# Optimization experiments

Hardware: AMD Instinct MI355X
Metric: run time of the kernel (lower is better)

The kernel has to match this reference:

```python
import jax, jax.numpy as jnp
import numpy as np

K = 3  # == stride, neighbors per token


def setup_inputs() -> dict:
    key = jax.random.key(0)
    k1, k2, k3 = jax.random.split(key, 3)
    x = jax.random.normal(k1, (16, 64, 2048), dtype=jnp.float32)        # (B, C, T)
    W = jax.random.normal(k2, (64, 64, K), dtype=jnp.float32) * 0.05     # (O, I, K) conv1d weight
    b = jax.random.normal(k3, (64,), dtype=jnp.float32) * 0.05           # (O,) conv1d bias
    return {"x": x, "W": W, "b": b}


def reference(x, W, b):
    B, C, T = x.shape
    # pairwise squared euclidean distances over the channel dim: (B, T, T)
    nsq = jnp.sum(x * x, axis=1)                       # (B, T)
    dot = jnp.einsum('bct,bcs->bts', x, x)             # (B, T, T)
    dist = jnp.maximum(nsq[:, :, None] + nsq[:, None, :] - 2.0 * dot, 0.0)
    # K nearest neighbors (smallest distance -> top_k of negated dist)
    _, idx = jax.lax.top_k(-dist, K)                   # (B, T, K) int32 indices
    # gather neighbor features: prime[b, c, i*K + k] = x[b, c, idx[b, i, k]]
    idx_flat = idx.reshape(B, 1, T * K)
    prime = jnp.take_along_axis(x, jnp.broadcast_to(idx_flat, (B, C, T * K)), axis=2)
    # Conv1d with kernel_size=K, stride=K, padding=0 -> output length T
    out = jax.lax.conv_general_dilated(
        prime, W, window_strides=(K,), padding='VALID',
        dimension_numbers=('NCH', 'OIH', 'NCH'))
    return out + b[None, :, None]
```

## Files before the change

### kernel.cpp

```cpp
#include <hip/hip_runtime.h>

#define B_ 16
#define C_ 64
#define T_ 2048
#define O_ 64
#define KNN 3
#define HSPLIT 2
#define JCH (T_ / HSPLIT)

typedef short short8   __attribute__((ext_vector_type(8)));
typedef float f32x4    __attribute__((ext_vector_type(4)));
typedef unsigned short ushortx4 __attribute__((ext_vector_type(4)));

#define XT_OFF 0
#define XS_OFF (XT_OFF + B_ * T_ * C_)
#define NSQ_OFF (XS_OFF + B_ * T_ * C_)
#define WT_OFF (NSQ_OFF + B_ * T_)
#define CAND_OFF (WT_OFF + 192 * O_)

__device__ inline ushort bf16_rne(float f) {
    union { float f; unsigned u; } cv; cv.f = f;
    unsigned u = cv.u;
    u += 0x7FFF + ((u >> 16) & 1);
    return (ushort)(u >> 16);
}
__device__ inline float bf16_val(ushort h) {
    union { unsigned u; float f; } cv; cv.u = ((unsigned)h) << 16; return cv.f;
}

__global__ __launch_bounds__(256) void prep_kernel(const float* __restrict__ x,
                                                   const float* __restrict__ W,
                                                   float* __restrict__ ws) {
    float*  xT  = ws + XT_OFF;
    ushort* xs  = (ushort*)(ws + XS_OFF);
    float*  nsq = ws + NSQ_OFF;
    float*  Wt  = ws + WT_OFF;
    int blk = blockIdx.x;
    int tid = threadIdx.x;
    if (blk < B_ * (T_ / 64)) {
        int b  = blk / (T_ / 64);
        int t0 = (blk % (T_ / 64)) * 64;
        __shared__ float tl[64 * 65];
        #pragma unroll
        for (int r = 0; r < 16; ++r) {
            int e = r * 256 + tid;
            int c = e >> 6, t = e & 63;
            tl[c * 65 + t] = x[(b * C_ + c) * T_ + t0 + t];
        }
        __syncthreads();
        #pragma unroll
        for (int r = 0; r < 16; ++r) {
            int e = r * 256 + tid;
            int t = e >> 6, c = e & 63;
            float v = tl[c * 65 + t];
            size_t rowg = (size_t)(b * T_ + t0 + t);
            xT[rowg * 64 + c] = v;
            ushort hi = bf16_rne(v);
            float  fr = v - bf16_val(hi);
            ushort lo = bf16_rne(fr);
            xs[rowg * 128 + c]      = hi;
            xs[rowg * 128 + 64 + c] = lo;
        }
        if (tid < 64) {
            float s = 0.f;
            #pragma unroll
            for (int c = 0; c < 64; ++c) { float v = tl[c * 65 + tid]; s = fmaf(v, v, s); }
            nsq[b * T_ + t0 + tid] = s;
        }
    } else {
        int e = (blk - B_ * (T_ / 64)) * 256 + tid;
        if (e < O_ * C_ * KNN) {
            int o = e / (C_ * KNN);
            int c = (e / KNN) % C_;
            int k = e % KNN;
            Wt[(k * 64 + c) * O_ + o] = W[e];
        }
    }
}

__global__ __launch_bounds__(256, 4) void knn_mfma_kernel(const ushort* __restrict__ xs,
                                                          const float* __restrict__ nsq,
                                                          ushort* __restrict__ cand) {
    __shared__ __align__(16) ushort jbuf[2][32 * 128];
    __shared__ float nsqs[JCH];

    int bid = blockIdx.x;
    int g   = bid & 31;
    int m   = bid >> 5;
    int b   = g >> 1, h = g & 1;
    int i0  = m * 128;
    int tid = threadIdx.x;
    int w   = tid >> 6, l = tid & 63, lr = l & 15, lq = l >> 4;
    const ushort* xsb = xs + (size_t)b * T_ * 128;
    int jBase = h * JCH;

    ((float4*)nsqs)[tid] = ((const float4*)(nsq + b * T_ + jBase))[tid];

    short8 bA0, bA1, bA4, bA5, bB0, bB1, bB4, bB5;
    {
        const ushort* ia = xsb + (size_t)(i0 + w * 32 + lr) * 128 + lq * 8;
        bA0 = *(const short8*)(ia + 0);  bA1 = *(const short8*)(ia + 32);
        bA4 = *(const short8*)(ia + 64); bA5 = *(const short8*)(ia + 96);
        const ushort* ib2 = ia + 16 * 128;
        bB0 = *(const short8*)(ib2 + 0);  bB1 = *(const short8*)(ib2 + 32);
        bB4 = *(const short8*)(ib2 + 64); bB5 = *(const short8*)(ib2 + 96);
    }
    float niA = nsq[b * T_ + i0 + w * 32 + lr] + 4.0f;
    float niB = nsq[b * T_ + i0 + w * 32 + 16 + lr] + 4.0f;

    const float INF = __builtin_inff();
    float kA0 = INF, kA1 = INF, kA2 = INF, kA3 = INF;
    float kB0 = INF, kB1 = INF, kB2 = INF, kB3 = INF;

    int cSw = lr ^ (w * 4 + lq);
    #define ISSUE_DMA(jsv, bufv) {                                               \
        _Pragma("unroll")                                                        \
        for (int p = 0; p < 2; ++p) {                                            \
            int rloc = p * 16 + w * 4 + lq;                                      \
            const ushort* gp = xsb + (size_t)(jBase + (jsv) * 32 + rloc) * 128 + cSw * 8; \
            __builtin_amdgcn_global_load_lds(                                    \
                (const __attribute__((address_space(1))) void*)gp,               \
                (__attribute__((address_space(3))) void*)(jbuf[bufv] + (p * 16 + w * 4) * 128), \
                16, 0, 0);                                                       \
        } }

    ISSUE_DMA(0, 0);

    #pragma unroll 1
    for (int js = 0; js < 32; ++js) {
        asm volatile("s_waitcnt vmcnt(0)" ::: "memory");
        __syncthreads();
        if (js < 31) ISSUE_DMA(js + 1, (js + 1) & 1);
        const char* jb8 = (const char*)jbuf[js & 1];
        #pragma unroll
        for (int tile = 0; tile < 2; ++tile) {
            const char* rowp = jb8 + (tile * 16 + lr) * 256;
            short8 ah0 = *(const short8*)(rowp + ((( 0 + lq) ^ lr) << 4));
            short8 ah1 = *(const short8*)(rowp + ((( 4 + lq) ^ lr) << 4));
            short8 al0 = *(const short8*)(rowp + ((( 8 + lq) ^ lr) << 4));
            short8 al1 = *(const short8*)(rowp + (((12 + lq) ^ lr) << 4));
            f32x4 accA = {0.f, 0.f, 0.f, 0.f};
            f32x4 accB = {0.f, 0.f, 0.f, 0.f};
            accA = __builtin_amdgcn_mfma_f32_16x16x32_bf16(ah0, bA0, accA, 0, 0, 0);
            accB = __builtin_amdgcn_mfma_f32_16x16x32_bf16(ah0, bB0, accB, 0, 0, 0);
            accA = __builtin_amdgcn_mfma_f32_16x16x32_bf16(ah1, bA1, accA, 0, 0, 0);
            accB = __builtin_amdgcn_mfma_f32_16x16x32_bf16(ah1, bB1, accB, 0, 0, 0);
            accA = __builtin_amdgcn_mfma_f32_16x16x32_bf16(al0, bA0, accA, 0, 0, 0);
            accB = __builtin_amdgcn_mfma_f32_16x16x32_bf16(al0, bB0, accB, 0, 0, 0);
            accA = __builtin_amdgcn_mfma_f32_16x16x32_bf16(al1, bA1, accA, 0, 0, 0);
            accB = __builtin_amdgcn_mfma_f32_16x16x32_bf16(al1, bB1, accB, 0, 0, 0);
            accA = __builtin_amdgcn_mfma_f32_16x16x32_bf16(ah0, bA4, accA, 0, 0, 0);
            accB = __builtin_amdgcn_mfma_f32_16x16x32_bf16(ah0, bB4, accB, 0, 0, 0);
            accA = __builtin_amdgcn_mfma_f32_16x16x32_bf16(ah1, bA5, accA, 0, 0, 0);
            accB = __builtin_amdgcn_mfma_f32_16x16x32_bf16(ah1, bB5, accB, 0, 0, 0);
            float4 nv = *(const float4*)(nsqs + js * 32 + tile * 16 + lq * 4);
            int idb = ((js * 2 + tile) << 2) | (lq << 8);
            #define INS(K0, K1, K2, K3, sv, idv) {                                  \
                unsigned uu = (__float_as_uint(sv) & 0xFFFFFC00u) | (unsigned)(idv); \
                float kf = __uint_as_float(uu);                                      \
                float n0 = fminf(K0, kf);                                            \
                float n1 = __builtin_amdgcn_fmed3f(K0, K1, kf);                      \
                float n2 = __builtin_amdgcn_fmed3f(K1, K2, kf);                      \
                float n3 = __builtin_amdgcn_fmed3f(K2, K3, kf);                      \
                K0 = n0; K1 = n1; K2 = n2; K3 = n3; }
            {
                float s0 = fmaf(-2.f, accA[0], nv.x + niA); INS(kA0, kA1, kA2, kA3, s0, idb + 0);
                float s1 = fmaf(-2.f, accA[1], nv.y + niA); INS(kA0, kA1, kA2, kA3, s1, idb + 1);
                float s2 = fmaf(-2.f, accA[2], nv.z + niA); INS(kA0, kA1, kA2, kA3, s2, idb + 2);
                float s3 = fmaf(-2.f, accA[3], nv.w + niA); INS(kA0, kA1, kA2, kA3, s3, idb + 3);
            }
            {
                float s0 = fmaf(-2.f, accB[0], nv.x + niB); INS(kB0, kB1, kB2, kB3, s0, idb + 0);
                float s1 = fmaf(-2.f, accB[1], nv.y + niB); INS(kB0, kB1, kB2, kB3, s1, idb + 1);
                float s2 = fmaf(-2.f, accB[2], nv.z + niB); INS(kB0, kB1, kB2, kB3, s2, idb + 2);
                float s3 = fmaf(-2.f, accB[3], nv.w + niB); INS(kB0, kB1, kB2, kB3, s3, idb + 3);
            }
            #undef INS
        }
    }

    __syncthreads();
    float* fbuf = (float*)jbuf;
    {
        float* pa = fbuf + (w * 32 + lr) * 16 + lq * 4;
        pa[0] = kA0; pa[1] = kA1; pa[2] = kA2; pa[3] = kA3;
        float* pb = fbuf + (w * 32 + 16 + lr) * 16 + lq * 4;
        pb[0] = kB0; pb[1] = kB1; pb[2] = kB2; pb[3] = kB3;
    }
    __syncthreads();
    if (l < 32) {
        int rloc = w * 32 + l;
        const float* pr = fbuf + rloc * 16;
        float m0 = INF, m1 = INF, m2 = INF, m3 = INF;
        #pragma unroll
        for (int q2 = 0; q2 < 16; ++q2) {
            float kf = pr[q2];
            float n0 = fminf(m0, kf);
            float n1 = __builtin_amdgcn_fmed3f(m0, m1, kf);
            float n2 = __builtin_amdgcn_fmed3f(m1, m2, kf);
            float n3 = __builtin_amdgcn_fmed3f(m2, m3, kf);
            m0 = n0; m1 = n1; m2 = n2; m3 = n3;
        }
        ushortx4 cv;
        #define DEC(mf, slot) { unsigned u = __float_as_uint(mf) & 1023u;            \
            cv[slot] = (ushort)(jBase + (((u >> 2) & 63u) << 4) + ((u >> 8) << 2) + (u & 3)); }
        DEC(m0, 0); DEC(m1, 1); DEC(m2, 2); DEC(m3, 3);
        #undef DEC
        int row = b * T_ + i0 + rloc;
        *(ushortx4*)(cand + (size_t)row * 8 + h * 4) = cv;
    }
}

__global__ __launch_bounds__(256, 4) void conv_fused_kernel(const float* __restrict__ ws,
                                                            const float* __restrict__ bias,
                                                            float* __restrict__ out) {
    const float*  xT   = ws + XT_OFF;
    const float*  nsq  = ws + NSQ_OFF;
    const float*  Wt   = ws + WT_OFF;
    const ushort* cand = (const ushort*)(ws + CAND_OFF);

    __shared__ float g_s[192 * 32];
    __shared__ int   jsel3[32 * 3];

    int bb  = blockIdx.x >> 6;
    int i0  = (blockIdx.x & 63) * 32;
    int tid = threadIdx.x;
    int w = tid >> 6, l = tid & 63, qw = l >> 4, lr = l & 15;
    int bT = bb * T_;

    const float INF = __builtin_inff();
    #pragma unroll
    for (int it = 0; it < 2; ++it) {
        int rl  = w * 8 + it * 4 + qw;
        int row = bT + i0 + rl;
        float4 av = *(const float4*)(xT + (size_t)row * 64 + lr * 4);
        int jown = cand[(size_t)row * 8 + (lr & 7)];
        float D0 = INF, D1 = INF, D2 = INF;
        int   I0 = 0x7FFFFFFF, I1 = 0x7FFFFFFF, I2 = 0x7FFFFFFF;
        #pragma unroll
        for (int t = 0; t < 8; ++t) {
            int jt = __shfl(jown, (l & 48) + t, 64);
            float4 bv = *(const float4*)(xT + (size_t)(bT + jt) * 64 + lr * 4);
            float p = fmaf(bv.w, av.w, fmaf(bv.z, av.z, fmaf(bv.y, av.y, bv.x * av.x)));
            p += __shfl_xor(p, 1, 64);
            p += __shfl_xor(p, 2, 64);
            p += __shfl_xor(p, 4, 64);
            p += __shfl_xor(p, 8, 64);
            float s = nsq[bT + jt] - 2.f * p;
            bool lt2 = (s < D2) || (s == D2 && jt < I2);
            bool lt1 = (s < D1) || (s == D1 && jt < I1);
            bool lt0 = (s < D0) || (s == D0 && jt < I0);
            float nD2 = lt1 ? D1 : (lt2 ? s : D2); int nI2 = lt1 ? I1 : (lt2 ? jt : I2);
            float nD1 = lt0 ? D0 : (lt1 ? s : D1); int nI1 = lt0 ? I0 : (lt1 ? jt : I1);
            D2 = nD2; I2 = nI2; D1 = nD1; I1 = nI1;
            D0 = lt0 ? s : D0; I0 = lt0 ? jt : I0;
        }
        if (lr == 0) {
            jsel3[rl * 3 + 0] = I0; jsel3[rl * 3 + 1] = I1; jsel3[rl * 3 + 2] = I2;
        }
    }
    __syncthreads();

    if (tid < 96) {
        int k  = tid >> 5;
        int ip = tid & 31;
        int j  = jsel3[ip * 3 + k];
        const float4* src = (const float4*)(xT + (size_t)(bT + j) * 64);
        #pragma unroll
        for (int c4 = 0; c4 < 16; ++c4) {
            float4 v = src[c4];
            int mm = k * 64 + c4 * 4;
            g_s[(mm + 0) * 32 + ip] = v.x;
            g_s[(mm + 1) * 32 + ip] = v.y;
            g_s[(mm + 2) * 32 + ip] = v.z;
            g_s[(mm + 3) * 32 + ip] = v.w;
        }
    }
    __syncthreads();

    int oq = tid >> 4;
    int iq = tid & 15;
    float a0x = 0.f, a0y = 0.f, a1x = 0.f, a1y = 0.f;
    float a2x = 0.f, a2y = 0.f, a3x = 0.f, a3y = 0.f;
    #pragma unroll 4
    for (int mm = 0; mm < 192; ++mm) {
        float4 wv = *(const float4*)(Wt + mm * 64 + oq * 4);
        float2 gv = *(const float2*)(g_s + mm * 32 + iq * 2);
        a0x = fmaf(wv.x, gv.x, a0x); a0y = fmaf(wv.x, gv.y, a0y);
        a1x = fmaf(wv.y, gv.x, a1x); a1y = fmaf(wv.y, gv.y, a1y);
        a2x = fmaf(wv.z, gv.x, a2x); a2y = fmaf(wv.z, gv.y, a2y);
        a3x = fmaf(wv.w, gv.x, a3x); a3y = fmaf(wv.w, gv.y, a3y);
    }
    int o0 = oq * 4;
    float b0 = bias[o0], b1 = bias[o0 + 1], b2 = bias[o0 + 2], b3 = bias[o0 + 3];
    float2 r0; r0.x = a0x + b0; r0.y = a0y + b0;
    float2 r1; r1.x = a1x + b1; r1.y = a1y + b1;
    float2 r2; r2.x = a2x + b2; r2.y = a2y + b2;
    float2 r3; r3.x = a3x + b3; r3.y = a3y + b3;
    size_t ob = (size_t)(bb * O_ + o0) * T_ + i0 + iq * 2;
    *(float2*)(out + ob)          = r0;
    *(float2*)(out + ob + T_)     = r1;
    *(float2*)(out + ob + 2 * T_) = r2;
    *(float2*)(out + ob + 3 * T_) = r3;
}

extern "C" void kernel_launch(void* const* d_in, const int* in_sizes, int n_in,
                              void* d_out, int out_size, void* d_ws, size_t ws_size,
                              hipStream_t stream) {
    const float* x    = (const float*)d_in[0];
    const float* W    = (const float*)d_in[1];
    const float* bias = (const float*)d_in[2];
    float* out = (float*)d_out;
    float* ws  = (float*)d_ws;

    prep_kernel<<<B_ * (T_ / 64) + 48, 256, 0, stream>>>(x, W, ws);
    knn_mfma_kernel<<<512, 256, 0, stream>>>(
        (const ushort*)(ws + XS_OFF), ws + NSQ_OFF, (ushort*)(ws + CAND_OFF));
    conv_fused_kernel<<<B_ * 64, 256, 0, stream>>>(ws, bias, out);
}
```

Baseline: 139.6 us.

## Fuse KNN candidate search, refinement and conv into one kernel without split

Merges the MFMA KNN search and the conv kernel into a single mega kernel. Each block now scans all 2048 columns instead of half, keeping 8 candidates in shared memory rather than writing them to global. This removes the candidate round trip and one launch. In exchange the grid drops from 512 to 256 blocks, so fewer blocks are available to hide latency across the CUs. Shared memory per block also grows, and the conv stage is serialized over four sub-tiles per block.

```diff
diff --git a/kernel.cpp b/kernel.cpp
--- a/kernel.cpp
+++ b/kernel.cpp
@@ -5,8 +5,6 @@
 #define T_ 2048
 #define O_ 64
 #define KNN 3
-#define HSPLIT 2
-#define JCH (T_ / HSPLIT)
 
 typedef short short8   __attribute__((ext_vector_type(8)));
 typedef float f32x4    __attribute__((ext_vector_type(4)));
@@ -16,7 +14,6 @@
 #define XS_OFF (XT_OFF + B_ * T_ * C_)
 #define NSQ_OFF (XS_OFF + B_ * T_ * C_)
 #define WT_OFF (NSQ_OFF + B_ * T_)
-#define CAND_OFF (WT_OFF + 192 * O_)
 
 __device__ inline ushort bf16_rne(float f) {
     union { float f; unsigned u; } cv; cv.f = f;
@@ -78,23 +75,31 @@
     }
 }
 
-__global__ __launch_bounds__(256, 4) void knn_mfma_kernel(const ushort* __restrict__ xs,
-                                                          const float* __restrict__ nsq,
-                                                          ushort* __restrict__ cand) {
+__global__ __launch_bounds__(256) void mega_kernel(const float* __restrict__ ws_c,
+                                                   const float* __restrict__ bias,
+                                                   float* __restrict__ out) {
+    const float*  xT  = ws_c + XT_OFF;
+    const ushort* xs  = (const ushort*)(ws_c + XS_OFF);
+    const float*  nsq = ws_c + NSQ_OFF;
+    const float*  Wt  = ws_c + WT_OFF;
+
     __shared__ __align__(16) ushort jbuf[2][32 * 128];
-    __shared__ float nsqs[JCH];
+    __shared__ float  nsqs[T_];
+    __shared__ ushort jcand[128 * 8];
+    __shared__ int    jsel3[128 * 3];
+    __shared__ float  g_s[192 * 32];
 
     int bid = blockIdx.x;
-    int g   = bid & 31;
-    int m   = bid >> 5;
-    int b   = g >> 1, h = g & 1;
+    int b   = bid & 15;
+    int m   = bid >> 4;
     int i0  = m * 128;
     int tid = threadIdx.x;
     int w   = tid >> 6, l = tid & 63, lr = l & 15, lq = l >> 4;
     const ushort* xsb = xs + (size_t)b * T_ * 128;
-    int jBase = h * JCH;
-
-    ((float4*)nsqs)[tid] = ((const float4*)(nsq + b * T_ + jBase))[tid];
+    int bT = b * T_;
+
+    ((float4*)nsqs)[tid]       = ((const float4*)(nsq + bT))[tid];
+    ((float4*)nsqs)[tid + 256] = ((const float4*)(nsq + bT))[tid + 256];
 
     short8 bA0, bA1, bA4, bA5, bB0, bB1, bB4, bB5;
     {
@@ -105,8 +110,8 @@
         bB0 = *(const short8*)(ib2 + 0);  bB1 = *(const short8*)(ib2 + 32);
         bB4 = *(const short8*)(ib2 + 64); bB5 = *(const short8*)(ib2 + 96);
     }
-    float niA = nsq[b * T_ + i0 + w * 32 + lr] + 4.0f;
-    float niB = nsq[b * T_ + i0 + w * 32 + 16 + lr] + 4.0f;
+    float niA = nsq[bT + i0 + w * 32 + lr] + 4.0f;
+    float niB = nsq[bT + i0 + w * 32 + 16 + lr] + 4.0f;
 
     const float INF = __builtin_inff();
     float kA0 = INF, kA1 = INF, kA2 = INF, kA3 = INF;
@@ -117,7 +122,7 @@
         _Pragma("unroll")                                                        \
         for (int p = 0; p < 2; ++p) {                                            \
             int rloc = p * 16 + w * 4 + lq;                                      \
-            const ushort* gp = xsb + (size_t)(jBase + (jsv) * 32 + rloc) * 128 + cSw * 8; \
+            const ushort* gp = xsb + (size_t)((jsv) * 32 + rloc) * 128 + cSw * 8; \
             __builtin_amdgcn_global_load_lds(                                    \
                 (const __attribute__((address_space(1))) void*)gp,               \
                 (__attribute__((address_space(3))) void*)(jbuf[bufv] + (p * 16 + w * 4) * 128), \
@@ -127,10 +132,10 @@
     ISSUE_DMA(0, 0);
 
     #pragma unroll 1
-    for (int js = 0; js < 32; ++js) {
+    for (int js = 0; js < 64; ++js) {
         asm volatile("s_waitcnt vmcnt(0)" ::: "memory");
         __syncthreads();
-        if (js < 31) ISSUE_DMA(js + 1, (js + 1) & 1);
+        if (js < 63) ISSUE_DMA(js + 1, (js + 1) & 1);
         const char* jb8 = (const char*)jbuf[js & 1];
         #pragma unroll
         for (int tile = 0; tile < 2; ++tile) {
@@ -154,9 +159,9 @@
             accA = __builtin_amdgcn_mfma_f32_16x16x32_bf16(ah1, bA5, accA, 0, 0, 0);
             accB = __builtin_amdgcn_mfma_f32_16x16x32_bf16(ah1, bB5, accB, 0, 0, 0);
             float4 nv = *(const float4*)(nsqs + js * 32 + tile * 16 + lq * 4);
-            int idb = ((js * 2 + tile) << 2) | (lq << 8);
+            int idb = ((js * 2 + tile) << 2) | (lq << 9);
             #define INS(K0, K1, K2, K3, sv, idv) {                                  \
-                unsigned uu = (__float_as_uint(sv) & 0xFFFFFC00u) | (unsigned)(idv); \
+                unsigned uu = (__float_as_uint(sv) & 0xFFFFF800u) | (unsigned)(idv); \
                 float kf = __uint_as_float(uu);                                      \
                 float n0 = fminf(K0, kf);                                            \
                 float n1 = __builtin_amdgcn_fmed3f(K0, K1, kf);                      \
@@ -192,6 +197,7 @@
         int rloc = w * 32 + l;
         const float* pr = fbuf + rloc * 16;
         float m0 = INF, m1 = INF, m2 = INF, m3 = INF;
+        float m4 = INF, m5 = INF, m6 = INF, m7 = INF;
         #pragma unroll
         for (int q2 = 0; q2 < 16; ++q2) {
             float kf = pr[q2];
@@ -199,42 +205,29 @@
             float n1 = __builtin_amdgcn_fmed3f(m0, m1, kf);
             float n2 = __builtin_amdgcn_fmed3f(m1, m2, kf);
             float n3 = __builtin_amdgcn_fmed3f(m2, m3, kf);
+            float n4 = __builtin_amdgcn_fmed3f(m3, m4, kf);
+            float n5 = __builtin_amdgcn_fmed3f(m4, m5, kf);
+            float n6 = __builtin_amdgcn_fmed3f(m5, m6, kf);
+            float n7 = __builtin_amdgcn_fmed3f(m6, m7, kf);
             m0 = n0; m1 = n1; m2 = n2; m3 = n3;
-        }
-        ushortx4 cv;
-        #define DEC(mf, slot) { unsigned u = __float_as_uint(mf) & 1023u;            \
-            cv[slot] = (ushort)(jBase + (((u >> 2) & 63u) << 4) + ((u >> 8) << 2) + (u & 3)); }
+            m4 = n4; m5 = n5; m6 = n6; m7 = n7;
+        }
+        ushort* dst = jcand + rloc * 8;
+        #define DEC(mf, slot) { unsigned u = __float_as_uint(mf) & 2047u;            \
+            dst[slot] = (ushort)((((u >> 2) & 127u) << 4) + ((u >> 9) << 2) + (u & 3)); }
         DEC(m0, 0); DEC(m1, 1); DEC(m2, 2); DEC(m3, 3);
+        DEC(m4, 4); DEC(m5, 5); DEC(m6, 6); DEC(m7, 7);
         #undef DEC
-        int row = b * T_ + i0 + rloc;
-        *(ushortx4*)(cand + (size_t)row * 8 + h * 4) = cv;
-    }
-}
-
-__global__ __launch_bounds__(256, 4) void conv_fused_kernel(const float* __restrict__ ws,
-                                                            const float* __restrict__ bias,
-                                                            float* __restrict__ out) {
-    const float*  xT   = ws + XT_OFF;
-    const float*  nsq  = ws + NSQ_OFF;
-    const float*  Wt   = ws + WT_OFF;
-    const ushort* cand = (const ushort*)(ws + CAND_OFF);
-
-    __shared__ float g_s[192 * 32];
-    __shared__ int   jsel3[32 * 3];
-
-    int bb  = blockIdx.x >> 6;
-    int i0  = (blockIdx.x & 63) * 32;
-    int tid = threadIdx.x;
-    int w = tid >> 6, l = tid & 63, qw = l >> 4, lr = l & 15;
-    int bT = bb * T_;
-
-    const float INF = __builtin_inff();
-    #pragma unroll
-    for (int it = 0; it < 2; ++it) {
-        int rl  = w * 8 + it * 4 + qw;
+    }
+    __syncthreads();
+
+    int qw = lq;
+    #pragma unroll 1
+    for (int pass = 0; pass < 8; ++pass) {
+        int rl  = pass * 16 + w * 4 + qw;
         int row = bT + i0 + rl;
         float4 av = *(const float4*)(xT + (size_t)row * 64 + lr * 4);
-        int jown = cand[(size_t)row * 8 + (lr & 7)];
+        int jown = jcand[rl * 8 + (lr & 7)];
         float D0 = INF, D1 = INF, D2 = INF;
         int   I0 = 0x7FFFFFFF, I1 = 0x7FFFFFFF, I2 = 0x7FFFFFFF;
         #pragma unroll
@@ -261,47 +254,52 @@
     }
     __syncthreads();
 
-    if (tid < 96) {
-        int k  = tid >> 5;
-        int ip = tid & 31;
-        int j  = jsel3[ip * 3 + k];
-        const float4* src = (const float4*)(xT + (size_t)(bT + j) * 64);
-        #pragma unroll
-        for (int c4 = 0; c4 < 16; ++c4) {
-            float4 v = src[c4];
-            int mm = k * 64 + c4 * 4;
-            g_s[(mm + 0) * 32 + ip] = v.x;
-            g_s[(mm + 1) * 32 + ip] = v.y;
-            g_s[(mm + 2) * 32 + ip] = v.z;
-            g_s[(mm + 3) * 32 + ip] = v.w;
-        }
-    }
-    __syncthreads();
-
-    int oq = tid >> 4;
-    int iq = tid & 15;
-    float a0x = 0.f, a0y = 0.f, a1x = 0.f, a1y = 0.f;
-    float a2x = 0.f, a2y = 0.f, a3x = 0.f, a3y = 0.f;
-    #pragma unroll 4
-    for (int mm = 0; mm < 192; ++mm) {
-        float4 wv = *(const float4*)(Wt + mm * 64 + oq * 4);
-        float2 gv = *(const float2*)(g_s + mm * 32 + iq * 2);
-        a0x = fmaf(wv.x, gv.x, a0x); a0y = fmaf(wv.x, gv.y, a0y);
-        a1x = fmaf(wv.y, gv.x, a1x); a1y = fmaf(wv.y, gv.y, a1y);
-        a2x = fmaf(wv.z, gv.x, a2x); a2y = fmaf(wv.z, gv.y, a2y);
-        a3x = fmaf(wv.w, gv.x, a3x); a3y = fmaf(wv.w, gv.y, a3y);
-    }
-    int o0 = oq * 4;
-    float b0 = bias[o0], b1 = bias[o0 + 1], b2 = bias[o0 + 2], b3 = bias[o0 + 3];
-    float2 r0; r0.x = a0x + b0; r0.y = a0y + b0;
-    float2 r1; r1.x = a1x + b1; r1.y = a1y + b1;
-    float2 r2; r2.x = a2x + b2; r2.y = a2y + b2;
-    float2 r3; r3.x = a3x + b3; r3.y = a3y + b3;
-    size_t ob = (size_t)(bb * O_ + o0) * T_ + i0 + iq * 2;
-    *(float2*)(out + ob)          = r0;
-    *(float2*)(out + ob + T_)     = r1;
-    *(float2*)(out + ob + 2 * T_) = r2;
-    *(float2*)(out + ob + 3 * T_) = r3;
+    #pragma unroll 1
+    for (int st = 0; st < 4; ++st) {
+        if (tid < 96) {
+            int k  = tid >> 5;
+            int ip = tid & 31;
+            int j  = jsel3[(st * 32 + ip) * 3 + k];
+            const float4* src = (const float4*)(xT + (size_t)(bT + j) * 64);
+            #pragma unroll
+            for (int c4 = 0; c4 < 16; ++c4) {
+                float4 v = src[c4];
+                int mm = k * 64 + c4 * 4;
+                g_s[(mm + 0) * 32 + ip] = v.x;
+                g_s[(mm + 1) * 32 + ip] = v.y;
+                g_s[(mm + 2) * 32 + ip] = v.z;
+                g_s[(mm + 3) * 32 + ip] = v.w;
+            }
+        }
+        __syncthreads();
+
+        int oq = tid >> 4;
+        int iq = tid & 15;
+        float a0x = 0.f, a0y = 0.f, a1x = 0.f, a1y = 0.f;
+        float a2x = 0.f, a2y = 0.f, a3x = 0.f, a3y = 0.f;
+        #pragma unroll 4
+        for (int mm = 0; mm < 192; ++mm) {
+            float4 wv = *(const float4*)(Wt + mm * 64 + oq * 4);
+            float2 gv = *(const float2*)(g_s + mm * 32 + iq * 2);
+            a0x = fmaf(wv.x, gv.x, a0x); a0y = fmaf(wv.x, gv.y, a0y);
+            a1x = fmaf(wv.y, gv.x, a1x); a1y = fmaf(wv.y, gv.y, a1y);
+            a2x = fmaf(wv.z, gv.x, a2x); a2y = fmaf(wv.z, gv.y, a2y);
+            a3x = fmaf(wv.w, gv.x, a3x); a3y = fmaf(wv.w, gv.y, a3y);
+        }
+        int o0 = oq * 4;
+        float b0 = bias[o0], b1 = bias[o0 + 1], b2 = bias[o0 + 2], b3 = bias[o0 + 3];
+        float2 r0; r0.x = a0x + b0; r0.y = a0y + b0;
+        float2 r1; r1.x = a1x + b1; r1.y = a1y + b1;
+        float2 r2; r2.x = a2x + b2; r2.y = a2y + b2;
+        float2 r3; r3.x = a3x + b3; r3.y = a3y + b3;
+        size_t ob = (size_t)(b * O_ + o0) * T_ + i0 + st * 32 + iq * 2;
+        *(float2*)(out + ob)          = r0;
+        *(float2*)(out + ob + T_)     = r1;
+        *(float2*)(out + ob + 2 * T_) = r2;
+        *(float2*)(out + ob + 3 * T_) = r3;
+        __syncthreads();
+    }
+    #undef ISSUE_DMA
 }
 
 extern "C" void kernel_launch(void* const* d_in, const int* in_sizes, int n_in,
@@ -314,7 +312,5 @@
     float* ws  = (float*)d_ws;
 
     prep_kernel<<<B_ * (T_ / 64) + 48, 256, 0, stream>>>(x, W, ws);
-    knn_mfma_kernel<<<512, 256, 0, stream>>>(
-        (const ushort*)(ws + XS_OFF), ws + NSQ_OFF, (ushort*)(ws + CAND_OFF));
-    conv_fused_kernel<<<B_ * 64, 256, 0, stream>>>(ws, bias, out);
-}
+    mega_kernel<<<256, 256, 0, stream>>>(ws, bias, out);
+}
```

Measured after the change: 183.6 us. 1.32x slower.

## Split KNN candidate search four ways and load j-tiles directly from global

Applied to the files above, without the earlier changes.

The j dimension is now split into four chunks instead of two, which doubles the KNN grid and produces 16 candidates per row instead of 8. The conv kernel's refinement loop grows to match. The double-buffered LDS DMA pipeline with its per-step waitcnt and barrier is dropped. Each wave now reads its B-operand fragments straight from global memory, relying on L2/L1 caching. This removes the sync overhead and increases parallelism, but it costs more redundant global loads and twice the exact-distance refinement work.

```diff
diff --git a/kernel.cpp b/kernel.cpp
--- a/kernel.cpp
+++ b/kernel.cpp
@@ -5,7 +5,7 @@
 #define T_ 2048
 #define O_ 64
 #define KNN 3
-#define HSPLIT 2
+#define HSPLIT 4
 #define JCH (T_ / HSPLIT)
 
 typedef short short8   __attribute__((ext_vector_type(8)));
@@ -81,20 +81,21 @@
 __global__ __launch_bounds__(256, 4) void knn_mfma_kernel(const ushort* __restrict__ xs,
                                                           const float* __restrict__ nsq,
                                                           ushort* __restrict__ cand) {
-    __shared__ __align__(16) ushort jbuf[2][32 * 128];
     __shared__ float nsqs[JCH];
+    __shared__ float fbuf[128 * 16];
 
     int bid = blockIdx.x;
-    int g   = bid & 31;
-    int m   = bid >> 5;
-    int b   = g >> 1, h = g & 1;
+    int g   = bid & 63;
+    int m   = bid >> 6;
+    int b   = g >> 2, h = g & 3;
     int i0  = m * 128;
     int tid = threadIdx.x;
     int w   = tid >> 6, l = tid & 63, lr = l & 15, lq = l >> 4;
     const ushort* xsb = xs + (size_t)b * T_ * 128;
     int jBase = h * JCH;
-
-    ((float4*)nsqs)[tid] = ((const float4*)(nsq + b * T_ + jBase))[tid];
+    int bT = b * T_;
+
+    ((float2*)nsqs)[tid] = ((const float2*)(nsq + bT + jBase))[tid];
 
     short8 bA0, bA1, bA4, bA5, bB0, bB1, bB4, bB5;
     {
@@ -105,82 +106,62 @@
         bB0 = *(const short8*)(ib2 + 0);  bB1 = *(const short8*)(ib2 + 32);
         bB4 = *(const short8*)(ib2 + 64); bB5 = *(const short8*)(ib2 + 96);
     }
-    float niA = nsq[b * T_ + i0 + w * 32 + lr] + 4.0f;
-    float niB = nsq[b * T_ + i0 + w * 32 + 16 + lr] + 4.0f;
+    float niA = nsq[bT + i0 + w * 32 + lr] + 4.0f;
+    float niB = nsq[bT + i0 + w * 32 + 16 + lr] + 4.0f;
 
     const float INF = __builtin_inff();
     float kA0 = INF, kA1 = INF, kA2 = INF, kA3 = INF;
     float kB0 = INF, kB1 = INF, kB2 = INF, kB3 = INF;
 
-    int cSw = lr ^ (w * 4 + lq);
-    #define ISSUE_DMA(jsv, bufv) {                                               \
-        _Pragma("unroll")                                                        \
-        for (int p = 0; p < 2; ++p) {                                            \
-            int rloc = p * 16 + w * 4 + lq;                                      \
-            const ushort* gp = xsb + (size_t)(jBase + (jsv) * 32 + rloc) * 128 + cSw * 8; \
-            __builtin_amdgcn_global_load_lds(                                    \
-                (const __attribute__((address_space(1))) void*)gp,               \
-                (__attribute__((address_space(3))) void*)(jbuf[bufv] + (p * 16 + w * 4) * 128), \
-                16, 0, 0);                                                       \
-        } }
-
-    ISSUE_DMA(0, 0);
-
-    #pragma unroll 1
-    for (int js = 0; js < 32; ++js) {
-        asm volatile("s_waitcnt vmcnt(0)" ::: "memory");
-        __syncthreads();
-        if (js < 31) ISSUE_DMA(js + 1, (js + 1) & 1);
-        const char* jb8 = (const char*)jbuf[js & 1];
-        #pragma unroll
-        for (int tile = 0; tile < 2; ++tile) {
-            const char* rowp = jb8 + (tile * 16 + lr) * 256;
-            short8 ah0 = *(const short8*)(rowp + ((( 0 + lq) ^ lr) << 4));
-            short8 ah1 = *(const short8*)(rowp + ((( 4 + lq) ^ lr) << 4));
-            short8 al0 = *(const short8*)(rowp + ((( 8 + lq) ^ lr) << 4));
-            short8 al1 = *(const short8*)(rowp + (((12 + lq) ^ lr) << 4));
-            f32x4 accA = {0.f, 0.f, 0.f, 0.f};
-            f32x4 accB = {0.f, 0.f, 0.f, 0.f};
-            accA = __builtin_amdgcn_mfma_f32_16x16x32_bf16(ah0, bA0, accA, 0, 0, 0);
-            accB = __builtin_amdgcn_mfma_f32_16x16x32_bf16(ah0, bB0, accB, 0, 0, 0);
-            accA = __builtin_amdgcn_mfma_f32_16x16x32_bf16(ah1, bA1, accA, 0, 0, 0);
-            accB = __builtin_amdgcn_mfma_f32_16x16x32_bf16(ah1, bB1, accB, 0, 0, 0);
-            accA = __builtin_amdgcn_mfma_f32_16x16x32_bf16(al0, bA0, accA, 0, 0, 0);
-            accB = __builtin_amdgcn_mfma_f32_16x16x32_bf16(al0, bB0, accB, 0, 0, 0);
-            accA = __builtin_amdgcn_mfma_f32_16x16x32_bf16(al1, bA1, accA, 0, 0, 0);
-            accB = __builtin_amdgcn_mfma_f32_16x16x32_bf16(al1, bB1, accB, 0, 0, 0);
-            accA = __builtin_amdgcn_mfma_f32_16x16x32_bf16(ah0, bA4, accA, 0, 0, 0);
-            accB = __builtin_amdgcn_mfma_f32_16x16x32_bf16(ah0, bB4, accB, 0, 0, 0);
-            accA = __builtin_amdgcn_mfma_f32_16x16x32_bf16(ah1, bA5, accA, 0, 0, 0);
-            accB = __builtin_amdgcn_mfma_f32_16x16x32_bf16(ah1, bB5, accB, 0, 0, 0);
-            float4 nv = *(const float4*)(nsqs + js * 32 + tile * 16 + lq * 4);
-            int idb = ((js * 2 + tile) << 2) | (lq << 8);
-            #define INS(K0, K1, K2, K3, sv, idv) {                                  \
-                unsigned uu = (__float_as_uint(sv) & 0xFFFFFC00u) | (unsigned)(idv); \
-                float kf = __uint_as_float(uu);                                      \
-                float n0 = fminf(K0, kf);                                            \
-                float n1 = __builtin_amdgcn_fmed3f(K0, K1, kf);                      \
-                float n2 = __builtin_amdgcn_fmed3f(K1, K2, kf);                      \
-                float n3 = __builtin_amdgcn_fmed3f(K2, K3, kf);                      \
-                K0 = n0; K1 = n1; K2 = n2; K3 = n3; }
-            {
-                float s0 = fmaf(-2.f, accA[0], nv.x + niA); INS(kA0, kA1, kA2, kA3, s0, idb + 0);
-                float s1 = fmaf(-2.f, accA[1], nv.y + niA); INS(kA0, kA1, kA2, kA3, s1, idb + 1);
-                float s2 = fmaf(-2.f, accA[2], nv.z + niA); INS(kA0, kA1, kA2, kA3, s2, idb + 2);
-                float s3 = fmaf(-2.f, accA[3], nv.w + niA); INS(kA0, kA1, kA2, kA3, s3, idb + 3);
-            }
-            {
-                float s0 = fmaf(-2.f, accB[0], nv.x + niB); INS(kB0, kB1, kB2, kB3, s0, idb + 0);
-                float s1 = fmaf(-2.f, accB[1], nv.y + niB); INS(kB0, kB1, kB2, kB3, s1, idb + 1);
-                float s2 = fmaf(-2.f, accB[2], nv.z + niB); INS(kB0, kB1, kB2, kB3, s2, idb + 2);
-                float s3 = fmaf(-2.f, accB[3], nv.w + niB); INS(kB0, kB1, kB2, kB3, s3, idb + 3);
-            }
-            #undef INS
-        }
-    }
-
-    __syncthreads();
-    float* fbuf = (float*)jbuf;
+    __syncthreads();
+
+    #pragma unroll 2
+    for (int jt16 = 0; jt16 < JCH / 16; ++jt16) {
+        const ushort* ar = xsb + (size_t)(jBase + jt16 * 16 + lr) * 128 + lq * 8;
+        short8 ah0 = *(const short8*)(ar + 0);
+        short8 ah1 = *(const short8*)(ar + 32);
+        short8 al0 = *(const short8*)(ar + 64);
+        short8 al1 = *(const short8*)(ar + 96);
+        f32x4 accA = {0.f, 0.f, 0.f, 0.f};
+        f32x4 accB = {0.f, 0.f, 0.f, 0.f};
+        accA = __builtin_amdgcn_mfma_f32_16x16x32_bf16(ah0, bA0, accA, 0, 0, 0);
+        accB = __builtin_amdgcn_mfma_f32_16x16x32_bf16(ah0, bB0, accB, 0, 0, 0);
+        accA = __builtin_amdgcn_mfma_f32_16x16x32_bf16(ah1, bA1, accA, 0, 0, 0);
+        accB = __builtin_amdgcn_mfma_f32_16x16x32_bf16(ah1, bB1, accB, 0, 0, 0);
+        accA = __builtin_amdgcn_mfma_f32_16x16x32_bf16(al0, bA0, accA, 0, 0, 0);
+        accB = __builtin_amdgcn_mfma_f32_16x16x32_bf16(al0, bB0, accB, 0, 0, 0);
+        accA = __builtin_amdgcn_mfma_f32_16x16x32_bf16(al1, bA1, accA, 0, 0, 0);
+        accB = __builtin_amdgcn_mfma_f32_16x16x32_bf16(al1, bB1, accB, 0, 0, 0);
+        accA = __builtin_amdgcn_mfma_f32_16x16x32_bf16(ah0, bA4, accA, 0, 0, 0);
+        accB = __builtin_amdgcn_mfma_f32_16x16x32_bf16(ah0, bB4, accB, 0, 0, 0);
+        accA = __builtin_amdgcn_mfma_f32_16x16x32_bf16(ah1, bA5, accA, 0, 0, 0);
+        accB = __builtin_amdgcn_mfma_f32_16x16x32_bf16(ah1, bB5, accB, 0, 0, 0);
+        float4 nv = *(const float4*)(nsqs + jt16 * 16 + lq * 4);
+        int idb = (jt16 << 2) | (lq << 8);
+        #define INS(K0, K1, K2, K3, sv, idv) {                                  \
+            unsigned uu = (__float_as_uint(sv) & 0xFFFFFC00u) | (unsigned)(idv); \
+            float kf = __uint_as_float(uu);                                      \
+            float n0 = fminf(K0, kf);                                            \
+            float n1 = __builtin_amdgcn_fmed3f(K0, K1, kf);                      \
+            float n2 = __builtin_amdgcn_fmed3f(K1, K2, kf);                      \
+            float n3 = __builtin_amdgcn_fmed3f(K2, K3, kf);                      \
+            K0 = n0; K1 = n1; K2 = n2; K3 = n3; }
+        {
+            float s0 = fmaf(-2.f, accA[0], nv.x + niA); INS(kA0, kA1, kA2, kA3, s0, idb + 0);
+            float s1 = fmaf(-2.f, accA[1], nv.y + niA); INS(kA0, kA1, kA2, kA3, s1, idb + 1);
+            float s2 = fmaf(-2.f, accA[2], nv.z + niA); INS(kA0, kA1, kA2, kA3, s2, idb + 2);
+            float s3 = fmaf(-2.f, accA[3], nv.w + niA); INS(kA0, kA1, kA2, kA3, s3, idb + 3);
+        }
+        {
+            float s0 = fmaf(-2.f, accB[0], nv.x + niB); INS(kB0, kB1, kB2, kB3, s0, idb + 0);
+            float s1 = fmaf(-2.f, accB[1], nv.y + niB); INS(kB0, kB1, kB2, kB3, s1, idb + 1);
+            float s2 = fmaf(-2.f, accB[2], nv.z + niB); INS(kB0, kB1, kB2, kB3, s2, idb + 2);
+            float s3 = fmaf(-2.f, accB[3], nv.w + niB); INS(kB0, kB1, kB2, kB3, s3, idb + 3);
+        }
+        #undef INS
+    }
+
+    __syncthreads();
     {
         float* pa = fbuf + (w * 32 + lr) * 16 + lq * 4;
         pa[0] = kA0; pa[1] = kA1; pa[2] = kA2; pa[3] = kA3;
@@ -206,8 +187,8 @@
             cv[slot] = (ushort)(jBase + (((u >> 2) & 63u) << 4) + ((u >> 8) << 2) + (u & 3)); }
         DEC(m0, 0); DEC(m1, 1); DEC(m2, 2); DEC(m3, 3);
         #undef DEC
-        int row = b * T_ + i0 + rloc;
-        *(ushortx4*)(cand + (size_t)row * 8 + h * 4) = cv;
+        int row = bT + i0 + rloc;
+        *(ushortx4*)(cand + (size_t)row * 16 + h * 4) = cv;
     }
 }
 
@@ -234,11 +215,11 @@
         int rl  = w * 8 + it * 4 + qw;
         int row = bT + i0 + rl;
         float4 av = *(const float4*)(xT + (size_t)row * 64 + lr * 4);
-        int jown = cand[(size_t)row * 8 + (lr & 7)];
+        int jown = cand[(size_t)row * 16 + lr];
         float D0 = INF, D1 = INF, D2 = INF;
         int   I0 = 0x7FFFFFFF, I1 = 0x7FFFFFFF, I2 = 0x7FFFFFFF;
         #pragma unroll
-        for (int t = 0; t < 8; ++t) {
+        for (int t = 0; t < 16; ++t) {
             int jt = __shfl(jown, (l & 48) + t, 64);
             float4 bv = *(const float4*)(xT + (size_t)(bT + jt) * 64 + lr * 4);
             float p = fmaf(bv.w, av.w, fmaf(bv.z, av.z, fmaf(bv.y, av.y, bv.x * av.x)));
@@ -314,7 +295,7 @@
     float* ws  = (float*)d_ws;
 
     prep_kernel<<<B_ * (T_ / 64) + 48, 256, 0, stream>>>(x, W, ws);
-    knn_mfma_kernel<<<512, 256, 0, stream>>>(
+    knn_mfma_kernel<<<1024, 256, 0, stream>>>(
         (const ushort*)(ws + XS_OFF), ws + NSQ_OFF, (ushort*)(ws + CAND_OFF));
     conv_fused_kernel<<<B_ * 64, 256, 0, stream>>>(ws, bias, out);
 }
```

New measurement: 177.5 us. +27.2%, slower.
